# Optimization experiments

Measured on AMD Instinct MI355X. Metric: run time of the kernel, lower is better.

Reference implementation:

```python
import jax, jax.numpy as jnp
import numpy as np
from jax import lax

B, T, V, E, H, C = 16, 1024, 256, 512, 1024, 256


def lstm_layer(x, h0, c0, Wih, Whh, bih, bhh):
    """Single unidirectional LSTM layer, batch_first. x: (B,T,I). Returns (ys,(h,c)).
    Torch gate order: i, f, g, o. Input projection hoisted out of the scan (one big GEMM)."""
    xg = jnp.einsum('bti,gi->btg', x, Wih) + (bih + bhh)  # (B,T,4H)

    def step(carry, xt):
        h, c = carry
        gates = xt + h @ Whh.T
        i, f, g, o = jnp.split(gates, 4, axis=-1)
        c = jax.nn.sigmoid(f) * c + jax.nn.sigmoid(i) * jnp.tanh(g)
        h = jax.nn.sigmoid(o) * jnp.tanh(c)
        return (h, c), h

    (h, c), ys = lax.scan(step, (h0, c0), jnp.swapaxes(xg, 0, 1))
    return jnp.swapaxes(ys, 0, 1), h, c


def run_stack(emb_tokens, h0s, c0s, layers):
    """layers: list of (Wih, Whh, bih, bhh). h0s/c0s: (L,B,H)."""
    x = emb_tokens
    hs, cs = [], []
    for l, (Wih, Whh, bih, bhh) in enumerate(layers):
        x, h, c = lstm_layer(x, h0s[l], c0s[l], Wih, Whh, bih, bhh)
        hs.append(h)
        cs.append(c)
    return x, jnp.stack(hs), jnp.stack(cs)


def setup_inputs() -> dict:
    key = jax.random.key(0)
    ks = iter(jax.random.split(key, 32))
    s = 1.0 / np.sqrt(H)

    def u(shape):
        return jax.random.uniform(next(ks), shape, jnp.float32, -s, s)

    inp = {"x": jax.random.randint(next(ks), (B, T), 0, V)}
    inp["enc_emb"] = jax.random.normal(next(ks), (V, E), jnp.float32)
    inp["dec_emb"] = jax.random.normal(next(ks), (V, E), jnp.float32)
    for pre in ("enc", "dec"):
        for l in range(2):
            I = E if l == 0 else H
            inp[f"{pre}_Wih{l}"] = u((4 * H, I))
            inp[f"{pre}_Whh{l}"] = u((4 * H, H))
            inp[f"{pre}_bih{l}"] = u((4 * H,))
            inp[f"{pre}_bhh{l}"] = u((4 * H,))
    inp["out_W"] = u((C, H))
    inp["out_b"] = u((C,))
    return inp


def reference(x, enc_emb, dec_emb,
              enc_Wih0, enc_Whh0, enc_bih0, enc_bhh0,
              enc_Wih1, enc_Whh1, enc_bih1, enc_bhh1,
              dec_Wih0, dec_Whh0, dec_bih0, dec_bhh0,
              dec_Wih1, dec_Whh1, dec_bih1, dec_bhh1,
              out_W, out_b):
    enc_layers = [(enc_Wih0, enc_Whh0, enc_bih0, enc_bhh0),
                  (enc_Wih1, enc_Whh1, enc_bih1, enc_bhh1)]
    dec_layers = [(dec_Wih0, dec_Whh0, dec_bih0, dec_bhh0),
                  (dec_Wih1, dec_Whh1, dec_bih1, dec_bhh1)]
    L = len(enc_layers)
    z = jnp.zeros((L, x.shape[0], H), jnp.float32)
    # Encoder (dropout is identity at inference)
    _, h, c = run_stack(enc_emb[x], z, z, enc_layers)
    # Decoder with teacher forcing on the same tokens
    dec_out, _, _ = run_stack(dec_emb[x], h, c, dec_layers)
    logits = dec_out @ out_W.T + out_b  # (B,T,C)
    return jnp.swapaxes(logits, 1, 2)   # (B,C,T)
```

## Files before the change

### kernel.cpp

```cpp
#include <hip/hip_runtime.h>
#include <stdint.h>

#define B_  16
#define T_  1024
#define H_  1024
#define E_  512
#define V_  256
#define C_  256

typedef __bf16 bf16x8 __attribute__((ext_vector_type(8)));
typedef float  f32x4  __attribute__((ext_vector_type(4)));
typedef unsigned short u16;
typedef unsigned int   u32;
typedef unsigned long long u64;

__device__ __forceinline__ float bf2f(u16 u) {
  union { unsigned int i; float f; } v; v.i = ((unsigned int)u) << 16; return v.f;
}
__device__ __forceinline__ u16 f2bf(float f) {
  union { float f; unsigned int i; } v; v.f = f;
  unsigned int u = v.i;
  return (u16)((u + 0x7fffu + ((u >> 16) & 1u)) >> 16);
}
__device__ __forceinline__ bf16x8 ld_bf8(const u16* p) {
  uint4 v = *(const uint4*)p;
  return __builtin_bit_cast(bf16x8, v);
}
__device__ __forceinline__ bf16x8 ld_bf8_coh(const u16* p) {
  union { u64 q[2]; bf16x8 v; } r;
  r.q[0] = __hip_atomic_load((const u64*)p,     __ATOMIC_RELAXED, __HIP_MEMORY_SCOPE_AGENT);
  r.q[1] = __hip_atomic_load((const u64*)p + 1, __ATOMIC_RELAXED, __HIP_MEMORY_SCOPE_AGENT);
  return r.v;
}
__device__ __forceinline__ float sigm(float x) { return 1.f / (1.f + __expf(-x)); }

__device__ __forceinline__ bf16x8 ldw8(const void* W, size_t off, bool f32in) {
  if (f32in) {
    const float* p = (const float*)W + off;
    float4 a = *(const float4*)p;
    float4 b = *(const float4*)(p + 4);
    union { u16 s[8]; bf16x8 v; } r;
    r.s[0]=f2bf(a.x); r.s[1]=f2bf(a.y); r.s[2]=f2bf(a.z); r.s[3]=f2bf(a.w);
    r.s[4]=f2bf(b.x); r.s[5]=f2bf(b.y); r.s[6]=f2bf(b.z); r.s[7]=f2bf(b.w);
    return r.v;
  }
  return ld_bf8((const u16*)W + off);
}
__device__ __forceinline__ float ldb1(const void* p, int i, bool f32in) {
  return f32in ? ((const float*)p)[i] : bf2f(((const u16*)p)[i]);
}

__global__ void probe_k(const u16* __restrict__ s, int* __restrict__ flag) {
  if (threadIdx.x == 0) {
    int cnt = 0;
    for (int i = 0; i < 256; ++i) {
      int e = (s[i] >> 7) & 0xFF;
      if (e >= 124) ++cnt;
    }
    flag[0] = (cnt >= 16) ? 1 : 0;
  }
}

__global__ void cvt_k(const void* __restrict__ src, u16* __restrict__ dst, int n,
                      const int* __restrict__ flagp) {
  int i = blockIdx.x * blockDim.x + threadIdx.x;
  if (i >= n) return;
  if (*flagp) dst[i] = f2bf(((const float*)src)[i]);
  else        dst[i] = ((const u16*)src)[i];
}

struct PersistArgs {
  const int* tok;
  const u16 *eemb, *demb;
  const void *Wih[4], *Whh[4], *bih[4], *bhh[4];
  u16 *zslot;
  u16 *he0[2], *he1[2], *hd0[2], *hd1[2];
  u16 *seq;
  u32 *flags;
  const int *dflag;
};

struct PhaseP {
  const void *Wx, *Wh, *bi, *bh;
  const u16* emb;
  const int* tok;
  u16 *r0[2], *r1[2];
  const u16 *h0init, *h1init;
  u16* seq;
  u32 *flags;
  bool f32in, init_c;
  int c0, bid, tid;
  u32 gp0;
};

__device__ __forceinline__ void gbar(u32* flags, int bid, int tid, u32 gp) {
  __syncthreads();
  if (tid == 0)
    __hip_atomic_store(&flags[bid * 16], gp, __ATOMIC_RELAXED, __HIP_MEMORY_SCOPE_AGENT);
  if (tid < 256) {
    while (__hip_atomic_load(&flags[tid * 16], __ATOMIC_RELAXED, __HIP_MEMORY_SCOPE_AGENT) < gp)
      __builtin_amdgcn_s_sleep(2);
  }
  __syncthreads();
}

template<int LAYER>
__device__ u32 run_phase(const PhaseP& q, f32x4* red4, float* gbuf, float* cbuf,
                         float* bbuf) {
  constexpr int KX = LAYER ? 1024 : 512;
  constexpr int NX = KX / 256;
  const int tid = q.tid, w = tid >> 6, l = tid & 63;
  const int rr = l & 15, ksub = (l >> 4) * 8;

  bf16x8 BX[2][NX], BH[2][4];
  #pragma unroll
  for (int t = 0; t < 2; ++t) {
    const size_t row = (size_t)((t * 2 + (rr >> 3)) * 1024 + q.c0 + (rr & 7));
    #pragma unroll
    for (int it = 0; it < NX; ++it)
      BX[t][it] = ldw8(q.Wx, row * KX + w * (KX / 8) + it * 32 + ksub, q.f32in);
    #pragma unroll
    for (int it = 0; it < 4; ++it)
      BH[t][it] = ldw8(q.Wh, row * 1024 + w * 128 + it * 32 + ksub, q.f32in);
  }
  if (tid < 32) {
    const int row = (tid >> 3) * 1024 + q.c0 + (tid & 7);
    bbuf[tid] = ldb1(q.bi, row, q.f32in) + ldb1(q.bh, row, q.f32in);
  }
  if (q.init_c && tid < 128) cbuf[tid] = 0.f;
  __syncthreads();

  int tok_cur = (LAYER == 0) ? q.tok[rr * T_ + 0] : 0;
  u32 gp = q.gp0;

  for (int s = 0; s <= T_; ++s) {
    const bool active = (LAYER == 0) ? (s < T_) : (s >= 1);
    if (active) {
      const u16* xrow;
      const u16* hrow;
      if (LAYER == 0) {
        xrow = q.emb + (size_t)tok_cur * 512;
        hrow = (s == 0) ? (q.h0init + rr * H_) : (q.r0[(s - 1) & 1] + rr * H_);
      } else {
        xrow = q.r0[(s - 1) & 1] + rr * H_;
        hrow = (s == 1) ? (q.h1init + rr * H_) : (q.r1[s & 1] + rr * H_);
      }
      f32x4 a0 = {0.f,0.f,0.f,0.f}, a1 = {0.f,0.f,0.f,0.f};
      if (LAYER == 0) {
        #pragma unroll
        for (int it = 0; it < NX; ++it) {
          bf16x8 a = ld_bf8(xrow + w * (KX / 8) + it * 32 + ksub);
          a0 = __builtin_amdgcn_mfma_f32_16x16x32_bf16(a, BX[0][it], a0, 0, 0, 0);
          a1 = __builtin_amdgcn_mfma_f32_16x16x32_bf16(a, BX[1][it], a1, 0, 0, 0);
        }
      } else {
        #pragma unroll
        for (int it = 0; it < NX; ++it) {
          bf16x8 a = ld_bf8_coh(xrow + w * (KX / 8) + it * 32 + ksub);
          a0 = __builtin_amdgcn_mfma_f32_16x16x32_bf16(a, BX[0][it], a0, 0, 0, 0);
          a1 = __builtin_amdgcn_mfma_f32_16x16x32_bf16(a, BX[1][it], a1, 0, 0, 0);
        }
      }
      #pragma unroll
      for (int it = 0; it < 4; ++it) {
        bf16x8 a = ld_bf8_coh(hrow + w * 128 + it * 32 + ksub);
        a0 = __builtin_amdgcn_mfma_f32_16x16x32_bf16(a, BH[0][it], a0, 0, 0, 0);
        a1 = __builtin_amdgcn_mfma_f32_16x16x32_bf16(a, BH[1][it], a1, 0, 0, 0);
      }
      red4[(w * 2 + 0) * 64 + l] = a0;
      red4[(w * 2 + 1) * 64 + l] = a1;
    }
    if (LAYER == 0) {
      const int tn = (s + 1 < T_) ? (s + 1) : (T_ - 1);
      tok_cur = q.tok[rr * T_ + tn];
    }
    __syncthreads();
    if (active && tid < 128) {
      const int tt = tid >> 6, ll = tid & 63;
      f32x4 ssum = {0.f,0.f,0.f,0.f};
      #pragma unroll
      for (int w8 = 0; w8 < 8; ++w8) ssum += red4[(w8 * 2 + tt) * 64 + ll];
      const int n = ll & 15, gate = tt * 2 + (n >> 3), j = n & 7, mg = (ll >> 4) * 4;
      const float bsum = bbuf[gate * 8 + j];
      #pragma unroll
      for (int r = 0; r < 4; ++r) gbuf[(gate * 8 + j) * 17 + mg + r] = ssum[r] + bsum;
    }
    __syncthreads();
    if (active && tid < 128) {
      const int j = tid >> 4, m = tid & 15;
      const float iv = sigm(gbuf[(0  + j) * 17 + m]);
      const float fv = sigm(gbuf[(8  + j) * 17 + m]);
      const float gv = tanhf(gbuf[(16 + j) * 17 + m]);
      const float ov = sigm(gbuf[(24 + j) * 17 + m]);
      const float cn = fv * cbuf[j * 16 + m] + iv * gv;
      cbuf[j * 16 + m] = cn;
      const u16 hv = f2bf(ov * tanhf(cn));
      u16* outs = (LAYER == 0) ? q.r0[s & 1] : q.r1[(s - 1) & 1];
      __hip_atomic_store(outs + m * H_ + q.c0 + j, hv,
                         __ATOMIC_RELAXED, __HIP_MEMORY_SCOPE_AGENT);
      if (q.seq) {
        const int t = s - 1;
        __hip_atomic_store(q.seq + ((size_t)m * T_ + t) * H_ + q.c0 + j, hv,
                           __ATOMIC_RELAXED, __HIP_MEMORY_SCOPE_AGENT);
      }
    }
    gbar(q.flags, q.bid, tid, gp);
    ++gp;
  }
  return gp;
}

__global__ __launch_bounds__(512, 2) void persist_k(PersistArgs P) {
  __shared__ f32x4 red4[16 * 64];
  __shared__ float gbuf[544];
  __shared__ float cbuf[128];
  __shared__ float bbuf[32];
  const int bid = blockIdx.x, tid = threadIdx.x;
  const int layer = bid >> 7;
  const int c0 = (bid & 127) * 8;
  const bool f32in = (*P.dflag != 0);

  u32 gp = 1;
  for (int ph = 0; ph < 2; ++ph) {
    PhaseP q;
    const int wi = ph * 2 + layer;
    q.Wx = P.Wih[wi]; q.Wh = P.Whh[wi]; q.bi = P.bih[wi]; q.bh = P.bhh[wi];
    q.emb = ph ? P.demb : P.eemb;
    q.tok = P.tok;
    q.r0[0] = ph ? P.hd0[0] : P.he0[0]; q.r0[1] = ph ? P.hd0[1] : P.he0[1];
    q.r1[0] = ph ? P.hd1[0] : P.he1[0]; q.r1[1] = ph ? P.hd1[1] : P.he1[1];
    q.h0init = ph ? P.he0[1] : P.zslot;
    q.h1init = ph ? P.he1[1] : P.zslot;
    q.seq = (ph == 1 && layer == 1) ? P.seq : nullptr;
    q.flags = P.flags;
    q.f32in = f32in; q.init_c = (ph == 0);
    q.c0 = c0; q.bid = bid; q.tid = tid; q.gp0 = gp;
    gp = layer ? run_phase<1>(q, red4, gbuf, cbuf, bbuf)
               : run_phase<0>(q, red4, gbuf, cbuf, bbuf);
  }
}

__global__ __launch_bounds__(256) void logits_k(const u16* __restrict__ A,
                                                const u16* __restrict__ W,
                                                const u16* __restrict__ bias,
                                                void* __restrict__ out,
                                                const int* __restrict__ dflag) {
  const int wid  = blockIdx.x * 4 + (threadIdx.x >> 6);
  const int mt   = wid >> 4;
  const int nt   = wid & 15;
  const int lane = threadIdx.x & 63;
  const int l15  = lane & 15;
  const int quad = lane >> 4;
  const int ko   = quad * 8;
  const u16* arow = A + (size_t)(mt * 16 + l15) * H_;
  const u16* brow = W + (size_t)(nt * 16 + l15) * H_;
  f32x4 acc = {0.f,0.f,0.f,0.f};
  #pragma unroll 4
  for (int kk = 0; kk < H_; kk += 32) {
    acc = __builtin_amdgcn_mfma_f32_16x16x32_bf16(ld_bf8(arow + kk + ko),
                                                  ld_bf8(brow + kk + ko), acc, 0, 0, 0);
  }
  const int c  = nt * 16 + l15;
  const float bv = bf2f(bias[c]);
  const int f32out = *dflag;
  #pragma unroll
  for (int r = 0; r < 4; ++r) {
    const int m = mt * 16 + quad * 4 + r;
    const int b = m >> 10, t = m & 1023;
    const size_t idx = ((size_t)b * C_ + c) * T_ + t;
    const float v = acc[r] + bv;
    if (f32out) ((float*)out)[idx] = v;
    else        ((u16*)out)[idx]   = f2bf(v);
  }
}

extern "C" void kernel_launch(void* const* d_in, const int* in_sizes, int n_in,
                              void* d_out, int out_size, void* d_ws, size_t ws_size,
                              hipStream_t stream) {
  (void)in_sizes; (void)n_in; (void)out_size; (void)ws_size;

  const int* x = (const int*)d_in[0];

  char* ws = (char*)d_ws;
  u32* flags  = (u32*)ws;
  u16* zslot  = (u16*)(ws + 16384);
  int* dflag  = (int*)(ws + 49152);
  char* base  = ws + 49408;
  size_t ob = 0;
  u16* p_eemb = (u16*)(base + ob); ob += (size_t)V_ * E_ * 2;
  u16* p_demb = (u16*)(base + ob); ob += (size_t)V_ * E_ * 2;
  u16* p_outW = (u16*)(base + ob); ob += (size_t)C_ * H_ * 2;
  u16* p_outb = (u16*)(base + ob); ob += 512;
  u16* rings  = (u16*)(base + ob); ob += 8 * (size_t)B_ * H_ * 2;
  u16* seq    = (u16*)(base + ob); ob += (size_t)B_ * T_ * H_ * 2;
  const size_t SLOT = (size_t)B_ * H_;

  hipMemsetAsync(ws, 0, 49408, stream);

  probe_k<<<1, 64, 0, stream>>>((const u16*)d_in[5], dflag);

  cvt_k<<<(V_ * E_ + 255) / 256, 256, 0, stream>>>(d_in[1], p_eemb, V_ * E_, dflag);
  cvt_k<<<(V_ * E_ + 255) / 256, 256, 0, stream>>>(d_in[2], p_demb, V_ * E_, dflag);
  cvt_k<<<(C_ * H_ + 255) / 256, 256, 0, stream>>>(d_in[19], p_outW, C_ * H_, dflag);
  cvt_k<<<1, 256, 0, stream>>>(d_in[20], p_outb, C_, dflag);

  PersistArgs P;
  P.tok = x; P.eemb = p_eemb; P.demb = p_demb;
  for (int l = 0; l < 4; ++l) {
    P.Wih[l] = d_in[3 + 4 * l + 0];
    P.Whh[l] = d_in[3 + 4 * l + 1];
    P.bih[l] = d_in[3 + 4 * l + 2];
    P.bhh[l] = d_in[3 + 4 * l + 3];
  }
  P.zslot = zslot;
  P.he0[0] = rings + 0 * SLOT; P.he0[1] = rings + 1 * SLOT;
  P.he1[0] = rings + 2 * SLOT; P.he1[1] = rings + 3 * SLOT;
  P.hd0[0] = rings + 4 * SLOT; P.hd0[1] = rings + 5 * SLOT;
  P.hd1[0] = rings + 6 * SLOT; P.hd1[1] = rings + 7 * SLOT;
  P.seq = seq; P.flags = flags; P.dflag = dflag;

  persist_k<<<256, 512, 0, stream>>>(P);

  logits_k<<<4096, 256, 0, stream>>>(seq, p_outW, p_outb, d_out, dflag);
}
```

Before: 14.58 ms.

## Halve persistent grid to 128 blocks, each owning 16 hidden columns

The persistent LSTM kernel now runs 128 workgroups instead of 256, with each block computing all four gates for 16 hidden units. That doubles the weights held in registers and the MFMA work per block, but it halves the number of participants in the per-step grid barrier. The change also vectorizes the h stores to 64-bit, uses a fast exp-based tanh, and skips the final barrier. The cost is heavier register pressure and more serial work per block on the recurrent critical path.

```diff
diff --git a/kernel.cpp b/kernel.cpp
--- a/kernel.cpp
+++ b/kernel.cpp
@@ -33,6 +33,9 @@
   return r.v;
 }
 __device__ __forceinline__ float sigm(float x) { return 1.f / (1.f + __expf(-x)); }
+__device__ __forceinline__ float tanhfast(float x) {
+  return 1.f - 2.f / (__expf(2.f * x) + 1.f);
+}
 
 __device__ __forceinline__ bf16x8 ldw8(const void* W, size_t off, bool f32in) {
   if (f32in) {
@@ -88,7 +91,7 @@
   const u16 *h0init, *h1init;
   u16* seq;
   u32 *flags;
-  bool f32in, init_c;
+  bool f32in, init_c, last;
   int c0, bid, tid;
   u32 gp0;
 };
@@ -97,7 +100,7 @@
   __syncthreads();
   if (tid == 0)
     __hip_atomic_store(&flags[bid * 16], gp, __ATOMIC_RELAXED, __HIP_MEMORY_SCOPE_AGENT);
-  if (tid < 256) {
+  if (tid < 128) {
     while (__hip_atomic_load(&flags[tid * 16], __ATOMIC_RELAXED, __HIP_MEMORY_SCOPE_AGENT) < gp)
       __builtin_amdgcn_s_sleep(2);
   }
@@ -112,22 +115,25 @@
   const int tid = q.tid, w = tid >> 6, l = tid & 63;
   const int rr = l & 15, ksub = (l >> 4) * 8;
 
-  bf16x8 BX[2][NX], BH[2][4];
+  bf16x8 BX[4][NX], BH[4][4];
   #pragma unroll
-  for (int t = 0; t < 2; ++t) {
-    const size_t row = (size_t)((t * 2 + (rr >> 3)) * 1024 + q.c0 + (rr & 7));
+  for (int g = 0; g < 4; ++g) {
+    const size_t row = (size_t)(g * 1024 + q.c0 + rr);
     #pragma unroll
     for (int it = 0; it < NX; ++it)
-      BX[t][it] = ldw8(q.Wx, row * KX + w * (KX / 8) + it * 32 + ksub, q.f32in);
+      BX[g][it] = ldw8(q.Wx, row * KX + w * (KX / 8) + it * 32 + ksub, q.f32in);
     #pragma unroll
     for (int it = 0; it < 4; ++it)
-      BH[t][it] = ldw8(q.Wh, row * 1024 + w * 128 + it * 32 + ksub, q.f32in);
-  }
-  if (tid < 32) {
-    const int row = (tid >> 3) * 1024 + q.c0 + (tid & 7);
+      BH[g][it] = ldw8(q.Wh, row * 1024 + w * 128 + it * 32 + ksub, q.f32in);
+  }
+  if (tid < 64) {
+    const int row = (tid >> 4) * 1024 + q.c0 + (tid & 15);
     bbuf[tid] = ldb1(q.bi, row, q.f32in) + ldb1(q.bh, row, q.f32in);
   }
-  if (q.init_c && tid < 128) cbuf[tid] = 0.f;
+  if (q.init_c && tid < 64) {
+    #pragma unroll
+    for (int k = 0; k < 4; ++k) cbuf[k * 64 + tid] = 0.f;
+  }
   __syncthreads();
 
   int tok_cur = (LAYER == 0) ? q.tok[rr * T_ + 0] : 0;
@@ -145,65 +151,65 @@
         xrow = q.r0[(s - 1) & 1] + rr * H_;
         hrow = (s == 1) ? (q.h1init + rr * H_) : (q.r1[s & 1] + rr * H_);
       }
-      f32x4 a0 = {0.f,0.f,0.f,0.f}, a1 = {0.f,0.f,0.f,0.f};
-      if (LAYER == 0) {
+      bf16x8 ax[NX], ah[4];
+      #pragma unroll
+      for (int it = 0; it < NX; ++it)
+        ax[it] = (LAYER == 0) ? ld_bf8(xrow + w * (KX / 8) + it * 32 + ksub)
+                              : ld_bf8_coh(xrow + w * (KX / 8) + it * 32 + ksub);
+      #pragma unroll
+      for (int it = 0; it < 4; ++it)
+        ah[it] = ld_bf8_coh(hrow + w * 128 + it * 32 + ksub);
+      #pragma unroll
+      for (int g = 0; g < 4; ++g) {
+        f32x4 acc = {0.f, 0.f, 0.f, 0.f};
         #pragma unroll
-        for (int it = 0; it < NX; ++it) {
-          bf16x8 a = ld_bf8(xrow + w * (KX / 8) + it * 32 + ksub);
-          a0 = __builtin_amdgcn_mfma_f32_16x16x32_bf16(a, BX[0][it], a0, 0, 0, 0);
-          a1 = __builtin_amdgcn_mfma_f32_16x16x32_bf16(a, BX[1][it], a1, 0, 0, 0);
-        }
-      } else {
+        for (int it = 0; it < NX; ++it)
+          acc = __builtin_amdgcn_mfma_f32_16x16x32_bf16(ax[it], BX[g][it], acc, 0, 0, 0);
         #pragma unroll
-        for (int it = 0; it < NX; ++it) {
-          bf16x8 a = ld_bf8_coh(xrow + w * (KX / 8) + it * 32 + ksub);
-          a0 = __builtin_amdgcn_mfma_f32_16x16x32_bf16(a, BX[0][it], a0, 0, 0, 0);
-          a1 = __builtin_amdgcn_mfma_f32_16x16x32_bf16(a, BX[1][it], a1, 0, 0, 0);
-        }
+        for (int it = 0; it < 4; ++it)
+          acc = __builtin_amdgcn_mfma_f32_16x16x32_bf16(ah[it], BH[g][it], acc, 0, 0, 0);
+        red4[(w * 4 + g) * 64 + l] = acc;
       }
-      #pragma unroll
-      for (int it = 0; it < 4; ++it) {
-        bf16x8 a = ld_bf8_coh(hrow + w * 128 + it * 32 + ksub);
-        a0 = __builtin_amdgcn_mfma_f32_16x16x32_bf16(a, BH[0][it], a0, 0, 0, 0);
-        a1 = __builtin_amdgcn_mfma_f32_16x16x32_bf16(a, BH[1][it], a1, 0, 0, 0);
-      }
-      red4[(w * 2 + 0) * 64 + l] = a0;
-      red4[(w * 2 + 1) * 64 + l] = a1;
     }
     if (LAYER == 0) {
       const int tn = (s + 1 < T_) ? (s + 1) : (T_ - 1);
       tok_cur = q.tok[rr * T_ + tn];
     }
     __syncthreads();
-    if (active && tid < 128) {
-      const int tt = tid >> 6, ll = tid & 63;
-      f32x4 ssum = {0.f,0.f,0.f,0.f};
-      #pragma unroll
-      for (int w8 = 0; w8 < 8; ++w8) ssum += red4[(w8 * 2 + tt) * 64 + ll];
-      const int n = ll & 15, gate = tt * 2 + (n >> 3), j = n & 7, mg = (ll >> 4) * 4;
-      const float bsum = bbuf[gate * 8 + j];
-      #pragma unroll
-      for (int r = 0; r < 4; ++r) gbuf[(gate * 8 + j) * 17 + mg + r] = ssum[r] + bsum;
+    if (active && tid < 256) {
+      const int g = tid >> 6, ll = tid & 63;
+      f32x4 ssum = {0.f, 0.f, 0.f, 0.f};
+      #pragma unroll
+      for (int w8 = 0; w8 < 8; ++w8) ssum += red4[(w8 * 4 + g) * 64 + ll];
+      const int n = ll & 15, mg = (ll >> 4) * 4;
+      const float bsum = bbuf[g * 16 + n];
+      #pragma unroll
+      for (int r = 0; r < 4; ++r) gbuf[(g * 16 + n) * 17 + mg + r] = ssum[r] + bsum;
     }
     __syncthreads();
-    if (active && tid < 128) {
-      const int j = tid >> 4, m = tid & 15;
-      const float iv = sigm(gbuf[(0  + j) * 17 + m]);
-      const float fv = sigm(gbuf[(8  + j) * 17 + m]);
-      const float gv = tanhf(gbuf[(16 + j) * 17 + m]);
-      const float ov = sigm(gbuf[(24 + j) * 17 + m]);
-      const float cn = fv * cbuf[j * 16 + m] + iv * gv;
-      cbuf[j * 16 + m] = cn;
-      const u16 hv = f2bf(ov * tanhf(cn));
+    if (active && tid < 64) {
+      const int m = tid & 15, jg = tid >> 4;
+      union { u16 s4[4]; u64 q8; } hp;
+      #pragma unroll
+      for (int k = 0; k < 4; ++k) {
+        const int col = jg * 4 + k;
+        const float iv = sigm(gbuf[( 0 + col) * 17 + m]);
+        const float fv = sigm(gbuf[(16 + col) * 17 + m]);
+        const float gv = tanhfast(gbuf[(32 + col) * 17 + m]);
+        const float ov = sigm(gbuf[(48 + col) * 17 + m]);
+        const float cn = fv * cbuf[k * 64 + tid] + iv * gv;
+        cbuf[k * 64 + tid] = cn;
+        hp.s4[k] = f2bf(ov * tanhfast(cn));
+      }
       u16* outs = (LAYER == 0) ? q.r0[s & 1] : q.r1[(s - 1) & 1];
-      __hip_atomic_store(outs + m * H_ + q.c0 + j, hv,
+      __hip_atomic_store((u64*)(outs + m * H_ + q.c0 + jg * 4), hp.q8,
                          __ATOMIC_RELAXED, __HIP_MEMORY_SCOPE_AGENT);
       if (q.seq) {
         const int t = s - 1;
-        __hip_atomic_store(q.seq + ((size_t)m * T_ + t) * H_ + q.c0 + j, hv,
-                           __ATOMIC_RELAXED, __HIP_MEMORY_SCOPE_AGENT);
+        *(u64*)(q.seq + ((size_t)m * T_ + t) * H_ + q.c0 + jg * 4) = hp.q8;
       }
     }
+    if (q.last && s == T_) break;
     gbar(q.flags, q.bid, tid, gp);
     ++gp;
   }
@@ -211,13 +217,13 @@
 }
 
 __global__ __launch_bounds__(512, 2) void persist_k(PersistArgs P) {
-  __shared__ f32x4 red4[16 * 64];
-  __shared__ float gbuf[544];
-  __shared__ float cbuf[128];
-  __shared__ float bbuf[32];
+  __shared__ f32x4 red4[32 * 64];
+  __shared__ float gbuf[64 * 17];
+  __shared__ float cbuf[4 * 64];
+  __shared__ float bbuf[64];
   const int bid = blockIdx.x, tid = threadIdx.x;
-  const int layer = bid >> 7;
-  const int c0 = (bid & 127) * 8;
+  const int layer = bid >> 6;
+  const int c0 = (bid & 63) * 16;
   const bool f32in = (*P.dflag != 0);
 
   u32 gp = 1;
@@ -233,7 +239,7 @@
     q.h1init = ph ? P.he1[1] : P.zslot;
     q.seq = (ph == 1 && layer == 1) ? P.seq : nullptr;
     q.flags = P.flags;
-    q.f32in = f32in; q.init_c = (ph == 0);
+    q.f32in = f32in; q.init_c = (ph == 0); q.last = (ph == 1);
     q.c0 = c0; q.bid = bid; q.tid = tid; q.gp0 = gp;
     gp = layer ? run_phase<1>(q, red4, gbuf, cbuf, bbuf)
                : run_phase<0>(q, red4, gbuf, cbuf, bbuf);
@@ -319,7 +325,7 @@
   P.hd1[0] = rings + 6 * SLOT; P.hd1[1] = rings + 7 * SLOT;
   P.seq = seq; P.flags = flags; P.dflag = dflag;
 
-  persist_k<<<256, 512, 0, stream>>>(P);
+  persist_k<<<128, 512, 0, stream>>>(P);
 
   logits_k<<<4096, 256, 0, stream>>>(seq, p_outW, p_outb, d_out, dflag);
 }
```

Result: faster. 14.06 ms (-3.6%).
